# Performance work log

Hardware: AMD Instinct MI355X
Metric: run time of the kernel (lower is better)

The kernel has to match this reference:

```python
import jax, jax.numpy as jnp
import numpy as np

N_HEADS = 8
N_LAYERS = 2
LN_EPS = 1e-5


def _mha(x, Win, bin_, Wout, bout):
    # torch nn.MultiheadAttention, eval mode (dropout off). x: [b, s, d]
    b, s, d = x.shape
    dh = d // N_HEADS
    qkv = x @ Win.T + bin_                      # [b, s, 3d]
    q, k, v = jnp.split(qkv, 3, axis=-1)
    q = q.reshape(b, s, N_HEADS, dh)
    k = k.reshape(b, s, N_HEADS, dh)
    v = v.reshape(b, s, N_HEADS, dh)
    scores = jnp.einsum('bqhd,bkhd->bhqk', q, k) / jnp.sqrt(jnp.asarray(dh, x.dtype))
    attn = jax.nn.softmax(scores, axis=-1)
    o = jnp.einsum('bhqk,bkhd->bqhd', attn, v).reshape(b, s, d)
    return o @ Wout.T + bout


def _layer_norm(x, g, b):
    mu = jnp.mean(x, axis=-1, keepdims=True)
    var = jnp.mean(jnp.square(x - mu), axis=-1, keepdims=True)
    return (x - mu) * jax.lax.rsqrt(var + LN_EPS) * g + b


def _vertex_conv(feat, inc, prev, Win, bin_, Wout, bout, Wproj, ln_g, ln_b, alpha):
    # feat: [b,m,d], inc: [b,m,e]
    attn = _mha(feat, Win, bin_, Wout, bout)              # [b,m,d]
    scores = jnp.einsum('bme,bmd->bed', inc, attn)        # incidence aggregation
    w = jax.nn.softmax(scores, axis=1)                    # softmax over edges
    # fused form of einsum('bme,bmd->bmed') then einsum('bmed,bed->bed')
    edge = scores * w                                     # [b,e,d]
    edge = edge @ Wproj.T                                 # no-bias projection
    edge = _layer_norm(edge, ln_g, ln_b)
    if prev is not None:
        edge = alpha * prev + (1.0 - alpha) * edge
        edge = edge + prev
    return edge


def _edge_conv(inc, edge_feat, prev, Win, bin_, Wout, bout, Wproj, ln_g, ln_b, alpha):
    # inc: [b,m,e], edge_feat: [b,e,d]
    _ = _mha(edge_feat, Win, bin_, Wout, bout)            # attn computed, output unused downstream
    wef = jnp.einsum('bed,bme->bmd', edge_feat, inc)      # edge->node aggregation
    node = wef @ Wproj.T
    node = _layer_norm(node, ln_g, ln_b)
    if prev is not None:
        node = alpha * prev + (1.0 - alpha) * node
        node = node + prev
    return node


def setup_inputs() -> dict:
    key = jax.random.key(0)
    ks = jax.random.split(key, 8)
    b, m, e, d = 8, 1024, 1536, 256
    s = 0.02
    return {
        'features': jax.random.normal(ks[0], (b, m, d), jnp.float32),
        'inc_mat': (jax.random.uniform(ks[1], (b, m, e), jnp.float32) < 0.05).astype(jnp.float32),
        'vc_Win': jax.random.normal(ks[2], (3 * d, d), jnp.float32) * s,
        'vc_bin': jnp.zeros((3 * d,), jnp.float32),
        'vc_Wout': jax.random.normal(ks[3], (d, d), jnp.float32) * s,
        'vc_bout': jnp.zeros((d,), jnp.float32),
        'vc_Wproj': jax.random.normal(ks[4], (d, d), jnp.float32) * s,
        'vc_ln_g': jnp.ones((d,), jnp.float32),
        'vc_ln_b': jnp.zeros((d,), jnp.float32),
        'vc_alpha': jnp.asarray(0.5, jnp.float32),
        'ec_Win': jax.random.normal(ks[5], (3 * d, d), jnp.float32) * s,
        'ec_bin': jnp.zeros((3 * d,), jnp.float32),
        'ec_Wout': jax.random.normal(ks[6], (d, d), jnp.float32) * s,
        'ec_bout': jnp.zeros((d,), jnp.float32),
        'ec_Wproj': jax.random.normal(ks[7], (d, d), jnp.float32) * s,
        'ec_ln_g': jnp.ones((d,), jnp.float32),
        'ec_ln_b': jnp.zeros((d,), jnp.float32),
        'ec_alpha': jnp.asarray(0.5, jnp.float32),
    }


def reference(features, inc_mat,
              vc_Win, vc_bin, vc_Wout, vc_bout, vc_Wproj, vc_ln_g, vc_ln_b, vc_alpha,
              ec_Win, ec_bin, ec_Wout, ec_bout, ec_Wproj, ec_ln_g, ec_ln_b, ec_alpha):
    vc = (vc_Win, vc_bin, vc_Wout, vc_bout, vc_Wproj, vc_ln_g, vc_ln_b, vc_alpha)
    ec = (ec_Win, ec_bin, ec_Wout, ec_bout, ec_Wproj, ec_ln_g, ec_ln_b, ec_alpha)
    edge_feats = _vertex_conv(features, inc_mat, None, *vc)
    node_feats = _edge_conv(inc_mat, edge_feats, features, *ec)
    for _ in range(N_LAYERS):  # shared weights across layers, as in the torch module
        edge_feats = _vertex_conv(features, inc_mat, edge_feats, *vc)
        node_feats = _edge_conv(inc_mat, edge_feats, node_feats, *ec)
    return node_feats, edge_feats, inc_mat
```

## Files before the change

### kernel.cpp

```cpp
#include <hip/hip_runtime.h>
#include <stdint.h>


#define DEV static __device__ __forceinline__

typedef __attribute__((ext_vector_type(8))) short bf16x8;
typedef __attribute__((ext_vector_type(4))) float f32x4;

DEV uint16_t f2bf(float x){
  union{float f; uint32_t u;} v; v.f=x;
  uint32_t r = v.u + 0x7fffu + ((v.u>>16)&1u);
  return (uint16_t)(r>>16);
}
DEV float bf2f(uint16_t b){
  union{uint32_t u; float f;} v; v.u=((uint32_t)b)<<16; return v.f;
}

DEV uint32_t cvtpk_bf16(float lo, float hi){
  uint32_t d;
  asm("v_cvt_pk_bf16_f32 %0, %1, %2" : "=v"(d) : "v"(lo), "v"(hi));
  return d;
}

#if __has_builtin(__builtin_amdgcn_exp2f)
DEV float exp2fast(float x){ return __builtin_amdgcn_exp2f(x); }
#else
DEV float exp2fast(float x){ return __expf(x * 0.6931471805599453f); }
#endif

#if __has_builtin(__builtin_amdgcn_global_load_lds)
#define HAVE_GLL 1
#else
#define HAVE_GLL 0
#endif

DEV void load_lds16(const uint16_t* g, void* l){
#if HAVE_GLL
  __builtin_amdgcn_global_load_lds((const __attribute__((address_space(1))) uint32_t*)g,
                                   (__attribute__((address_space(3))) uint32_t*)l, 16, 0, 0);
#else
  *(bf16x8*)l = *(const bf16x8*)g;
#endif
}

__global__ __launch_bounds__(256, 3)
void qkv_prep(const float* __restrict__ inc, float* __restrict__ out_inc,
              uint16_t* __restrict__ incb, uint16_t* __restrict__ incT,
              const float* __restrict__ feats, const float* __restrict__ win,
              const float* __restrict__ bias, uint16_t* __restrict__ qkvb,
              const float* __restrict__ wout, const float* __restrict__ wpv,
              const float* __restrict__ wpe,
              uint16_t* __restrict__ ob_w, uint16_t* __restrict__ ov_w,
              uint16_t* __restrict__ oe_w,
              float* __restrict__ incpart){
  __shared__ union {
    struct { short As[128*32]; short Bs[128*32]; } g;
    float T[64*65];
  } sm;
  const int tid = threadIdx.x;
  const int bx = blockIdx.x;

  if (bx < 384){
    const int lane = tid & 63;
    const int w = tid >> 6;
    const int wm = w & 1, wn = w >> 1;
    const int r = lane & 15, q = lane >> 4;
    const int mtile = bx & 63, ntile = bx >> 6;
    const float* Fb = feats + (size_t)(mtile*128)*256;
    const float* Wb = win + (size_t)(ntile*128)*256;
    f32x4 acc[4][4];
#pragma unroll
    for (int i=0;i<4;++i)
#pragma unroll
      for (int j=0;j<4;++j) acc[i][j] = (f32x4){0.f,0.f,0.f,0.f};

    const int srow = tid >> 2;
    const int sblk = tid & 3;

    for (int kb = 0; kb < 256; kb += 32){
#pragma unroll
      for (int i=0;i<2;++i){
        int row = srow + 64*i;
        const float* src = Fb + (size_t)row*256 + kb + sblk*8;
        float4 a0 = *(const float4*)src;
        float4 a1 = *(const float4*)(src+4);
        union{uint32_t u[4]; bf16x8 v8;} pk;
        pk.u[0]=cvtpk_bf16(a0.x,a0.y); pk.u[1]=cvtpk_bf16(a0.z,a0.w);
        pk.u[2]=cvtpk_bf16(a1.x,a1.y); pk.u[3]=cvtpk_bf16(a1.z,a1.w);
        *(bf16x8*)&sm.g.As[row*32 + (sblk ^ (row&3))*8] = pk.v8;
      }
#pragma unroll
      for (int i=0;i<2;++i){
        int row = srow + 64*i;
        const float* src = Wb + (size_t)row*256 + kb + sblk*8;
        float4 a0 = *(const float4*)src;
        float4 a1 = *(const float4*)(src+4);
        union{uint32_t u[4]; bf16x8 v8;} pk;
        pk.u[0]=cvtpk_bf16(a0.x,a0.y); pk.u[1]=cvtpk_bf16(a0.z,a0.w);
        pk.u[2]=cvtpk_bf16(a1.x,a1.y); pk.u[3]=cvtpk_bf16(a1.z,a1.w);
        *(bf16x8*)&sm.g.Bs[row*32 + (sblk ^ (row&3))*8] = pk.v8;
      }
      __syncthreads();
      bf16x8 af[4], bfr[4];
#pragma unroll
      for (int mt=0;mt<4;++mt){
        int m = wm*64 + mt*16 + r;
        af[mt] = *(const bf16x8*)&sm.g.As[m*32 + (q ^ (m&3))*8];
      }
#pragma unroll
      for (int nt=0;nt<4;++nt){
        int n = wn*64 + nt*16 + r;
        bfr[nt] = *(const bf16x8*)&sm.g.Bs[n*32 + (q ^ (n&3))*8];
      }
#pragma unroll
      for (int mt=0;mt<4;++mt)
#pragma unroll
        for (int nt=0;nt<4;++nt)
          acc[mt][nt] = __builtin_amdgcn_mfma_f32_16x16x32_bf16(af[mt], bfr[nt], acc[mt][nt], 0,0,0);
      __syncthreads();
    }

    const int gm0 = mtile*128 + wm*64;
    const int gn0 = ntile*128 + wn*64;
#pragma unroll
    for (int mt=0;mt<4;++mt){
#pragma unroll
      for (int nt=0;nt<4;++nt){
        int gn = gn0 + nt*16 + r;
        float bv = bias[gn];
#pragma unroll
        for (int reg=0;reg<4;++reg){
          int gm = gm0 + mt*16 + q*4 + reg;
          qkvb[(size_t)gm*768 + gn] = f2bf(acc[mt][nt][reg] + bv);
        }
      }
    }
  } else if (bx < 3456){
    int p = bx - 384;
    int x = p % 24;
    int t = p / 24;
    int y = t & 15;
    int b = t >> 4;
    int c0 = x*64, r0 = y*64;
    int tx = tid & 15, ty = tid >> 4;
    size_t base = (size_t)b*1024*1536;
#pragma unroll
    for (int jj=0;jj<4;++jj){
      int rl = ty + jj*16;
      size_t idx = base + (size_t)(r0+rl)*1536 + c0 + tx*4;
      float4 v = *(const float4*)&inc[idx];
      *(float4*)&out_inc[idx] = v;
      union{uint16_t u[4]; uint64_t q64;} pk;
      pk.u[0]=f2bf(v.x); pk.u[1]=f2bf(v.y); pk.u[2]=f2bf(v.z); pk.u[3]=f2bf(v.w);
      *(uint64_t*)&incb[idx] = pk.q64;
      float* Tp = &sm.T[rl*65 + tx*4];
      Tp[0]=v.x; Tp[1]=v.y; Tp[2]=v.z; Tp[3]=v.w;
    }
    __syncthreads();
    int c = tid >> 2, ms = (tid & 3) * 16;
    size_t baseT = (size_t)b*1536*1024;
    uint16_t* dst = incT + baseT + (size_t)(c0+c)*1024 + r0 + ms;
    union{uint16_t u[8]; uint4 v4;} o0, o1;
    float csum = 0.f;
#pragma unroll
    for (int j=0;j<8;++j){ float v = sm.T[(ms+j)*65 + c]; csum += v; o0.u[j] = f2bf(v); }
#pragma unroll
    for (int j=0;j<8;++j){ float v = sm.T[(ms+8+j)*65 + c]; csum += v; o1.u[j] = f2bf(v); }
    *(uint4*)dst = o0.v4;
    *(uint4*)(dst+8) = o1.v4;
    csum += __shfl_xor(csum, 1);
    csum += __shfl_xor(csum, 2);
    if ((tid & 3) == 0)
      incpart[((size_t)(b*16 + y))*1536 + c0 + c] = csum;
  } else {
    int i = (bx - 3456)*256 + tid;
    const float* src; uint16_t* dst; int j;
    if (i < 16384){ src=wout; dst=ob_w; j=i; }
    else if (i < 32768){ src=wpv; dst=ov_w; j=i-16384; }
    else { src=wpe; dst=oe_w; j=i-32768; }
    float4 v = ((const float4*)src)[j];
    union { uint16_t u[4]; uint64_t q; } p;
    p.u[0]=f2bf(v.x); p.u[1]=f2bf(v.y); p.u[2]=f2bf(v.z); p.u[3]=f2bf(v.w);
    ((uint64_t*)dst)[j] = p.q;
  }
}

__global__ __launch_bounds__(256, 3)
void gemm_score_fused(const uint16_t* __restrict__ A,
                      const uint16_t* __restrict__ OT,
                      const uint16_t* __restrict__ woutb,
                      const float* __restrict__ bout,
                      const float* __restrict__ incpart,
                      float* __restrict__ part,
                      uint16_t* __restrict__ VE){
  __shared__ short Ws[256*64];
  __shared__ short As[32*64];
  __shared__ short As2[32*256];
  __shared__ float incsum[32];
  const int tid = threadIdx.x;
  const int lane = tid & 63;
  const int w = tid >> 6;
  const int r = lane & 15, q = lane >> 4;
  const int bx = (blockIdx.x & 7)*48 + (blockIdx.x >> 3);
  const int batch = bx / 48;
  const int etile = bx % 48;

  if (tid < 32){
    float s = 0.f;
#pragma unroll
    for (int y=0;y<16;++y)
      s += incpart[((size_t)(batch*16 + y))*1536 + etile*32 + tid];
    incsum[tid] = s;
  }

  const uint16_t* Ab = A + (size_t)(batch*1536 + etile*32)*1024;
  const uint16_t* Bb = OT + (size_t)batch*256*1024;

  f32x4 acc1[4][2];
#pragma unroll
  for (int i=0;i<4;++i)
#pragma unroll
    for (int j=0;j<2;++j) acc1[i][j] = (f32x4){0.f,0.f,0.f,0.f};

  const int srow = tid >> 3;
  const int sblk = tid & 7;

  for (int kb = 0; kb < 1024; kb += 64){
#pragma unroll
    for (int i=0;i<8;++i){
      int row = srow + 32*i;
      int lblk = sblk ^ (row & 7);
      load_lds16(Bb + (size_t)row*1024 + kb + lblk*8, (char*)Ws + i*4096 + tid*16);
    }
    { int lblk = sblk ^ (srow & 7);
      load_lds16(Ab + (size_t)srow*1024 + kb + lblk*8, (char*)As + tid*16); }
    __syncthreads();
#pragma unroll
    for (int kc=0;kc<2;++kc){
      bf16x8 af[4], bfr[2];
#pragma unroll
      for (int mt=0;mt<4;++mt){
        int j = w*64 + mt*16 + r;
        af[mt] = *(const bf16x8*)&Ws[j*64 + ((kc*4 + q) ^ (j&7))*8];
      }
#pragma unroll
      for (int nt=0;nt<2;++nt){
        int e = nt*16 + r;
        bfr[nt] = *(const bf16x8*)&As[e*64 + ((kc*4 + q) ^ (e&7))*8];
      }
#pragma unroll
      for (int mt=0;mt<4;++mt)
#pragma unroll
        for (int nt=0;nt<2;++nt)
          acc1[mt][nt] = __builtin_amdgcn_mfma_f32_16x16x32_bf16(af[mt], bfr[nt], acc1[mt][nt], 0,0,0);
    }
    __syncthreads();
  }

#pragma unroll
  for (int mt=0;mt<4;++mt){
    int J = w*8 + mt*2 + (q>>1);
#pragma unroll
    for (int nt=0;nt<2;++nt){
      int e = nt*16 + r;
      union{uint16_t u[4]; uint64_t q64;} pk;
#pragma unroll
      for (int reg=0;reg<4;++reg) pk.u[reg] = f2bf(acc1[mt][nt][reg]);
      *(uint64_t*)((char*)As2 + e*512 + ((J ^ (e&7))<<4) + ((q&1)<<3)) = pk.q64;
    }
  }

  f32x4 acc2[4][2];
#pragma unroll
  for (int i=0;i<4;++i)
#pragma unroll
    for (int j=0;j<2;++j) acc2[i][j] = (f32x4){0.f,0.f,0.f,0.f};

  for (int kb = 0; kb < 256; kb += 64){
#pragma unroll
    for (int i=0;i<8;++i){
      int row = srow + 32*i;
      int lblk = sblk ^ (row & 7);
      load_lds16(woutb + (size_t)row*256 + kb + lblk*8, (char*)Ws + i*4096 + tid*16);
    }
    __syncthreads();
#pragma unroll
    for (int kc=0;kc<2;++kc){
      bf16x8 af[4], bfr[2];
#pragma unroll
      for (int mt=0;mt<4;++mt){
        int d = w*64 + mt*16 + r;
        af[mt] = *(const bf16x8*)&Ws[d*64 + ((kc*4 + q) ^ (d&7))*8];
      }
#pragma unroll
      for (int nt=0;nt<2;++nt){
        int e = nt*16 + r;
        int Jr = (kb>>3) + kc*4 + q;
        bfr[nt] = *(const bf16x8*)((char*)As2 + e*512 + ((Jr ^ (e&7))<<4));
      }
#pragma unroll
      for (int mt=0;mt<4;++mt)
#pragma unroll
        for (int nt=0;nt<2;++nt)
          acc2[mt][nt] = __builtin_amdgcn_mfma_f32_16x16x32_bf16(af[mt], bfr[nt], acc2[mt][nt], 0,0,0);
    }
    __syncthreads();
  }

#pragma unroll
  for (int mt=0;mt<4;++mt){
    int d0 = w*64 + mt*16 + q*4;
    float4 bo = *(const float4*)&bout[d0];
    float colsum[4] = {0.f,0.f,0.f,0.f};
#pragma unroll
    for (int nt=0;nt<2;++nt){
      int e = nt*16 + r;
      const float isum = incsum[e];
      size_t er = (size_t)batch*1536 + etile*32 + e;
      union{uint16_t u[4]; uint64_t q64;} pk;
#pragma unroll
      for (int reg=0;reg<4;++reg){
        float bvv = (reg==0)?bo.x:(reg==1)?bo.y:(reg==2)?bo.z:bo.w;
        float v = acc2[mt][nt][reg] + isum*bvv;
        float ev = __expf(v);
        colsum[reg] += ev;
        pk.u[reg] = f2bf(v*ev);
      }
      *(uint64_t*)(VE + er*256 + d0) = pk.q64;
    }
#pragma unroll
    for (int reg=0;reg<4;++reg){
      float s = colsum[reg];
      s += __shfl_xor(s, 1);
      s += __shfl_xor(s, 2);
      s += __shfl_xor(s, 4);
      s += __shfl_xor(s, 8);
      if (r == 0)
        part[((size_t)(batch*48 + etile))*256 + d0 + reg] = s;
    }
  }
}

__global__ __launch_bounds__(256, 4)
void gemm_ln_edge(const uint16_t* __restrict__ SB, const uint16_t* __restrict__ B,
                  const float* __restrict__ part, const float* __restrict__ g,
                  const float* __restrict__ bb, const float* __restrict__ alpha,
                  float* __restrict__ out, uint16_t* __restrict__ baset){
  __shared__ short As[16*64];
  __shared__ short Bs[256*64];
  __shared__ float lnS[4][16], lnQ[4][16];
  __shared__ float PLinv[256];
  const int tid = threadIdx.x;
  const int lane = tid & 63;
  const int w = tid >> 6;
  const int r = lane & 15, q = lane >> 4;
  const int bx = (blockIdx.x & 7)*96 + (blockIdx.x >> 3);
  const int batch = bx / 96;

  {
    float s = 0.f;
#pragma unroll
    for (int i=0;i<48;++i) s += part[((size_t)batch*48 + i)*256 + tid];
    PLinv[tid] = 1.0f / s;
  }
  __syncthreads();

  f32x4 acc[4];
#pragma unroll
  for (int j=0;j<4;++j) acc[j] = (f32x4){0.f,0.f,0.f,0.f};

  const int srow = tid >> 3;
  const int sblk = tid & 7;

  for (int kb = 0; kb < 256; kb += 64){
    if (tid < 128){
      bf16x8 v = *(const bf16x8*)(SB + (size_t)(bx*16 + srow)*256 + kb + sblk*8);
      const float* Lp = &PLinv[kb + sblk*8];
      float xv[8];
#pragma unroll
      for (int j=0;j<8;++j) xv[j] = bf2f((uint16_t)v[j]) * Lp[j];
      union{uint32_t u[4]; bf16x8 v8;} pk;
      pk.u[0] = cvtpk_bf16(xv[0], xv[1]);
      pk.u[1] = cvtpk_bf16(xv[2], xv[3]);
      pk.u[2] = cvtpk_bf16(xv[4], xv[5]);
      pk.u[3] = cvtpk_bf16(xv[6], xv[7]);
      *(bf16x8*)&As[srow*64 + (sblk ^ (srow&7))*8] = pk.v8;
    }
#pragma unroll
    for (int i=0;i<8;++i){
      int row = srow + 32*i;
      int lblk = sblk ^ (row & 7);
      load_lds16(B + (size_t)row*256 + kb + lblk*8, (char*)Bs + i*4096 + tid*16);
    }
    __syncthreads();
#pragma unroll
    for (int kc=0;kc<2;++kc){
      bf16x8 af, bfr[4];
      { int m = r;
        af = *(const bf16x8*)&As[m*64 + ((kc*4 + q) ^ (m&7))*8]; }
#pragma unroll
      for (int nt=0;nt<4;++nt){
        int n = w*64 + nt*16 + r;
        bfr[nt] = *(const bf16x8*)&Bs[n*64 + ((kc*4 + q) ^ (n&7))*8];
      }
#pragma unroll
      for (int nt=0;nt<4;++nt)
        acc[nt] = __builtin_amdgcn_mfma_f32_16x16x32_bf16(af, bfr[nt], acc[nt], 0,0,0);
    }
    __syncthreads();
  }

  float rs[4], rq[4];
#pragma unroll
  for (int reg=0;reg<4;++reg){
    float s=0.f, s2=0.f;
#pragma unroll
    for (int nt=0;nt<4;++nt){
      float v = acc[nt][reg];
      s += v; s2 += v*v;
    }
#pragma unroll
    for (int off=1; off<16; off<<=1){ s += __shfl_xor(s,off); s2 += __shfl_xor(s2,off); }
    rs[reg]=s; rq[reg]=s2;
  }
  if (r == 0){
#pragma unroll
    for (int reg=0;reg<4;++reg){
      int row = q*4 + reg;
      lnS[w][row] = rs[reg];
      lnQ[w][row] = rq[reg];
    }
  }
  __syncthreads();

  const float c0 = 3.0f + alpha[0];
  float mu_[4], rstd_[4];
#pragma unroll
  for (int reg=0;reg<4;++reg){
    int row = q*4 + reg;
    float S = lnS[0][row]+lnS[1][row]+lnS[2][row]+lnS[3][row];
    float Q = lnQ[0][row]+lnQ[1][row]+lnQ[2][row]+lnQ[3][row];
    float mu = S * (1.f/256.f);
    float var = fmaxf(Q*(1.f/256.f) - mu*mu, 0.f);
    mu_[reg] = mu;
    rstd_[reg] = rsqrtf(var + 1e-5f);
  }

  int e0 = (bx % 96) * 16;
#pragma unroll
  for (int nt=0;nt<4;++nt){
    int gn = w*64 + nt*16 + r;
    float gv = g[gn], bv = bb[gn];
    union{uint16_t u[4]; uint64_t q64;} pk;
#pragma unroll
    for (int reg=0;reg<4;++reg){
      int row = q*4 + reg;
      size_t gm = (size_t)bx*16 + row;
      float o = ((acc[nt][reg]-mu_[reg])*rstd_[reg]*gv + bv) * c0;
      pk.u[reg] = f2bf(o);
      out[gm*256 + gn] = o;
    }
    int ee = e0 + q*4;
    *(uint64_t*)(baset + ((size_t)batch*256 + gn)*1536 + ee) = pk.q64;
  }
}

__global__ __launch_bounds__(256, 3)
void gemm_node_fused(const uint16_t* __restrict__ inc,
                     const uint16_t* __restrict__ baset,
                     const uint16_t* __restrict__ wpe,
                     const float* __restrict__ g, const float* __restrict__ bb,
                     const float* __restrict__ alpha,
                     const float* __restrict__ feats, float* __restrict__ out){
  __shared__ short Ws[256*64];
  __shared__ short As2[16*256];
  __shared__ short Is[16*64];
  const int tid = threadIdx.x;
  const int lane = tid & 63;
  const int w = tid >> 6;
  const int r = lane & 15, q = lane >> 4;
  const int bx = (blockIdx.x & 7)*64 + (blockIdx.x >> 3);
  const int batch = bx >> 6;
  const int mt0 = (bx & 63) * 16;

  const int srow = tid >> 3;
  const int sblk = tid & 7;

  const uint16_t* Bb = baset + (size_t)batch*256*1536;
  const uint16_t* Ib = inc + ((size_t)batch*1024 + mt0)*1536;

  f32x4 acc1[4];
#pragma unroll
  for (int i=0;i<4;++i) acc1[i] = (f32x4){0.f,0.f,0.f,0.f};

  for (int kb = 0; kb < 1536; kb += 64){
#pragma unroll
    for (int i=0;i<8;++i){
      int row = srow + 32*i;
      int lblk = sblk ^ (row & 7);
      load_lds16(Bb + (size_t)row*1536 + kb + lblk*8, (char*)Ws + i*4096 + tid*16);
    }
    if (tid < 128){
      int lblk = sblk ^ (srow & 7);
      load_lds16(Ib + (size_t)srow*1536 + kb + lblk*8, (char*)Is + tid*16);
    }
    __syncthreads();
#pragma unroll
    for (int kc=0;kc<2;++kc){
      bf16x8 af[4], bfr;
#pragma unroll
      for (int mt=0;mt<4;++mt){
        int d = w*64 + mt*16 + r;
        af[mt] = *(const bf16x8*)&Ws[d*64 + ((kc*4 + q) ^ (d&7))*8];
      }
      { int m = r;
        bfr = *(const bf16x8*)&Is[m*64 + ((kc*4 + q) ^ (m&7))*8]; }
#pragma unroll
      for (int mt=0;mt<4;++mt)
        acc1[mt] = __builtin_amdgcn_mfma_f32_16x16x32_bf16(af[mt], bfr, acc1[mt], 0,0,0);
    }
    __syncthreads();
  }

#pragma unroll
  for (int mt=0;mt<4;++mt){
    int j = w*8 + mt*2 + (q>>1);
    int m = r;
    union{uint16_t u[4]; uint64_t q64;} pk;
#pragma unroll
    for (int reg=0;reg<4;++reg) pk.u[reg] = f2bf(acc1[mt][reg]);
    *(uint64_t*)((char*)As2 + m*512 + ((j ^ (m&7))<<4) + ((q&1)<<3)) = pk.q64;
  }

  f32x4 acc2[4];
#pragma unroll
  for (int i=0;i<4;++i) acc2[i] = (f32x4){0.f,0.f,0.f,0.f};

  for (int kb = 0; kb < 256; kb += 64){
#pragma unroll
    for (int i=0;i<8;++i){
      int row = srow + 32*i;
      int lblk = sblk ^ (row & 7);
      load_lds16(wpe + (size_t)row*256 + kb + lblk*8, (char*)Ws + i*4096 + tid*16);
    }
    __syncthreads();
#pragma unroll
    for (int kc=0;kc<2;++kc){
      bf16x8 af[4], bfr;
#pragma unroll
      for (int mt=0;mt<4;++mt){
        int dp = w*64 + mt*16 + r;
        af[mt] = *(const bf16x8*)&Ws[dp*64 + ((kc*4 + q) ^ (dp&7))*8];
      }
      { int m = r;
        int jr = (kb>>3) + kc*4 + q;
        bfr = *(const bf16x8*)((char*)As2 + m*512 + ((jr ^ (m&7))<<4)); }
#pragma unroll
      for (int mt=0;mt<4;++mt)
        acc2[mt] = __builtin_amdgcn_mfma_f32_16x16x32_bf16(af[mt], bfr, acc2[mt], 0,0,0);
    }
    __syncthreads();
  }

  float* lnS = (float*)Is;
  float* lnQ = lnS + 64;
  float s_, q_;
  {
    float s=0.f, s2=0.f;
#pragma unroll
    for (int mt=0;mt<4;++mt)
#pragma unroll
      for (int reg=0;reg<4;++reg){
        float v = acc2[mt][reg];
        s += v; s2 += v*v;
      }
    s += __shfl_xor(s,16); s2 += __shfl_xor(s2,16);
    s += __shfl_xor(s,32); s2 += __shfl_xor(s2,32);
    s_ = s; q_ = s2;
  }
  if (q == 0){
    lnS[w*16 + r] = s_;
    lnQ[w*16 + r] = q_;
  }
  __syncthreads();

  const float a = alpha[0];
  const float ap1 = 1.f + a;
  const float cn = (1.f - a)*(ap1*ap1 + ap1 + 1.f);
  const float cf = ap1*ap1*ap1;

  float mu_, rstd_;
  {
    int col = r;
    float S = lnS[col] + lnS[16+col] + lnS[32+col] + lnS[48+col];
    float Q = lnQ[col] + lnQ[16+col] + lnQ[32+col] + lnQ[48+col];
    float mu = S * (1.f/256.f);
    float var = fmaxf(Q*(1.f/256.f) - mu*mu, 0.f);
    mu_ = mu;
    rstd_ = rsqrtf(var + 1e-5f);
  }

#pragma unroll
  for (int mt=0;mt<4;++mt){
    int dp0 = w*64 + mt*16 + q*4;
    float4 gv = *(const float4*)&g[dp0];
    float4 bv = *(const float4*)&bb[dp0];
    int m = r;
    size_t gm = (size_t)batch*1024 + mt0 + m;
    float4 fv = *(const float4*)&feats[gm*256 + dp0];
    float4 ov;
    ov.x = cf*fv.x + cn*((acc2[mt][0]-mu_)*rstd_*gv.x + bv.x);
    ov.y = cf*fv.y + cn*((acc2[mt][1]-mu_)*rstd_*gv.y + bv.y);
    ov.z = cf*fv.z + cn*((acc2[mt][2]-mu_)*rstd_*gv.z + bv.z);
    ov.w = cf*fv.w + cn*((acc2[mt][3]-mu_)*rstd_*gv.w + bv.w);
    *(float4*)&out[gm*256 + dp0] = ov;
  }
}

DEV void stage_K(short* Kl, const uint16_t* __restrict__ qkv, size_t rowbase,
                 int c, int h, int kr){
  const uint16_t* kp = qkv + ((rowbase + c*256 + kr)*768 + 256 + h*32);
  int sz = (kr&3) ^ ((kr>>2)&1);
#pragma unroll
  for (int lb=0; lb<4; ++lb){
    bf16x8 v = *(const bf16x8*)(kp + lb*8);
    *(bf16x8*)&Kl[kr*32 + ((lb ^ sz))*8] = v;
  }
}

DEV void stage_V(short* VT, const uint16_t* __restrict__ qkv, size_t rowbase,
                 int c, int h, int t){
  int kvp = (t>>1)*2;
  int dhh = (t&1)*16;
  const uint16_t* v0 = qkv + ((rowbase + c*256 + kvp)*768 + 512 + h*32 + dhh);
  const uint16_t* v1 = v0 + 768;
  bf16x8 a0 = *(const bf16x8*)(v0);
  bf16x8 a1 = *(const bf16x8*)(v0+8);
  bf16x8 b0 = *(const bf16x8*)(v1);
  bf16x8 b1 = *(const bf16x8*)(v1+8);
  int blkbase = kvp>>3, off = kvp&7;
#pragma unroll
  for (int i=0;i<8;++i){
    int dh = dhh + i;
    uint32_t pack = (uint32_t)(uint16_t)a0[i] | ((uint32_t)(uint16_t)b0[i]<<16);
    *(uint32_t*)&VT[dh*256 + ((blkbase ^ (dh&7))*8) + off] = pack;
  }
#pragma unroll
  for (int i=0;i<8;++i){
    int dh = dhh + 8 + i;
    uint32_t pack = (uint32_t)(uint16_t)a1[i] | ((uint32_t)(uint16_t)b1[i]<<16);
    *(uint32_t*)&VT[dh*256 + ((blkbase ^ (dh&7))*8) + off] = pack;
  }
}

__global__ __launch_bounds__(512)
void attn_fwd(const uint16_t* __restrict__ qkv, uint16_t* __restrict__ OT){
  __shared__ short Kl[256*32];
  __shared__ short VT[32*256];
  __shared__ short Pl[8][16*36];
  const int tid = threadIdx.x, lane = tid&63, w = tid>>6;
  const int r = lane&15, q = lane>>4;
  const int logical = (blockIdx.x & 7)*64 + (blockIdx.x >> 3);
  const int bh = logical >> 3, qc = logical & 7;
  const int b = bh>>3, h = bh&7;
  const int q0 = qc*128 + w*16;
  const size_t rowbase = (size_t)b*1024;

  bf16x8 aq;
  {
    const float qscale = 0.25505654380651023f;
    const uint16_t* p = qkv + ((rowbase + q0 + r)*768 + h*32 + q*8);
    bf16x8 t = *(const bf16x8*)p;
#pragma unroll
    for (int j=0;j<8;++j)
      t[j] = (short)f2bf(bf2f((uint16_t)t[j]) * qscale);
    aq = t;
  }

  f32x4 o[2];
  o[0]=(f32x4){0.f,0.f,0.f,0.f}; o[1]=(f32x4){0.f,0.f,0.f,0.f};
  float l = 0.f;

  for (int c=0;c<4;++c){
    __syncthreads();
    if (tid < 256) stage_K(Kl, qkv, rowbase, c, h, tid);
    else           stage_V(VT, qkv, rowbase, c, h, tid-256);
    __syncthreads();
    for (int s32=0; s32<8; ++s32){
#pragma unroll
      for (int t2=0;t2<2;++t2){
        int rn = s32*32 + t2*16 + r;
        int sz = (rn&3) ^ ((rn>>2)&1);
        bf16x8 bk = *(const bf16x8*)&Kl[rn*32 + ((q ^ sz))*8];
        f32x4 z = (f32x4){0.f,0.f,0.f,0.f};
        __builtin_amdgcn_s_setprio(1);
        f32x4 st = __builtin_amdgcn_mfma_f32_16x16x32_bf16(bk, aq, z, 0,0,0);
        __builtin_amdgcn_s_setprio(0);
        float p0 = exp2fast(st[0]);
        float p1 = exp2fast(st[1]);
        float p2 = exp2fast(st[2]);
        float p3 = exp2fast(st[3]);
        l += (p0+p1)+(p2+p3);
        union{uint32_t u[2]; uint64_t q64;} pk;
        pk.u[0] = cvtpk_bf16(p0, p1);
        pk.u[1] = cvtpk_bf16(p2, p3);
        *(uint64_t*)&Pl[w][r*36 + t2*16 + q*4] = pk.q64;
      }
      bf16x8 bv[2];
#pragma unroll
      for (int db=0;db<2;++db){
        int dh = db*16 + r;
        bv[db] = *(const bf16x8*)&VT[dh*256 + (((s32*4 + q) ^ (dh&7)))*8];
      }
      bf16x8 ap = *(const bf16x8*)&Pl[w][r*36 + q*8];
      __builtin_amdgcn_s_setprio(1);
#pragma unroll
      for (int db=0;db<2;++db)
        o[db] = __builtin_amdgcn_mfma_f32_16x16x32_bf16(ap, bv[db], o[db], 0,0,0);
      __builtin_amdgcn_s_setprio(0);
    }
  }

  l += __shfl_xor(l, 16);
  l += __shfl_xor(l, 32);

  short* Ob = &Pl[0][0];
  __syncthreads();
#pragma unroll
  for (int db=0; db<2; ++db){
    union{uint16_t u[4]; uint64_t q64;} pk;
#pragma unroll
    for (int reg=0;reg<4;++reg){
      float li = __shfl(l, q*4 + reg);
      pk.u[reg] = f2bf(o[db][reg] / li);
    }
    int j = db*16 + r;
    int u = w*4 + q;
    *(uint64_t*)((char*)Ob + j*256 + ((u ^ ((j&7)<<2))<<3)) = pk.q64;
  }
  __syncthreads();
  {
    int row = tid >> 4, i = tid & 15;
    uint4 v = *(const uint4*)((char*)Ob + row*256 + (((2*i) ^ ((row&7)<<2))<<3));
    *(uint4*)&OT[((size_t)(b*256 + h*32 + row))*1024 + qc*128 + i*8] = v;
  }
}

extern "C" void kernel_launch(void* const* d_in, const int* in_sizes, int n_in,
                              void* d_out, int out_size, void* d_ws, size_t ws_size,
                              hipStream_t stream){
  const float* features = (const float*)d_in[0];
  const float* inc      = (const float*)d_in[1];
  const float* vc_Win   = (const float*)d_in[2];
  const float* vc_bin   = (const float*)d_in[3];
  const float* vc_Wout  = (const float*)d_in[4];
  const float* vc_bout  = (const float*)d_in[5];
  const float* vc_Wproj = (const float*)d_in[6];
  const float* vc_ln_g  = (const float*)d_in[7];
  const float* vc_ln_b  = (const float*)d_in[8];
  const float* vc_alpha = (const float*)d_in[9];
  const float* ec_Wproj = (const float*)d_in[14];
  const float* ec_ln_g  = (const float*)d_in[15];
  const float* ec_ln_b  = (const float*)d_in[16];
  const float* ec_alpha = (const float*)d_in[17];

  float* out = (float*)d_out;
  float* out_node = out;
  float* out_edge = out + 2097152;
  float* out_inc  = out + 5242880;

  char* ws = (char*)d_ws;
  float*    PART   = (float*)   (ws + 0);
  float*    INCPART= (float*)   (ws + 1048576);
  uint16_t* WOUTB  = (uint16_t*)(ws + 4587520);
  uint16_t* WPVB   = (uint16_t*)(ws + 4718592);
  uint16_t* WPEB   = (uint16_t*)(ws + 4849664);
  uint16_t* INCB   = (uint16_t*)(ws + 4988928);
  uint16_t* INCT   = (uint16_t*)(ws + 30154752);
  uint16_t* QKVB   = (uint16_t*)(ws + 55320576);
  uint16_t* SCORESB= (uint16_t*)(ws + 55320576);
  uint16_t* OT     = (uint16_t*)(ws + 67903488);
  uint16_t* BASET  = (uint16_t*)(ws + 82583552);

  qkv_prep<<<3648,256,0,stream>>>(inc, out_inc, INCB, INCT,
                                  features, vc_Win, vc_bin, QKVB,
                                  vc_Wout, vc_Wproj, ec_Wproj,
                                  WOUTB, WPVB, WPEB, INCPART);

  attn_fwd<<<512,512,0,stream>>>(QKVB, OT);

  gemm_score_fused<<<384,256,0,stream>>>(INCT, OT, WOUTB, vc_bout,
                                         INCPART, PART, SCORESB);

  gemm_ln_edge<<<768,256,0,stream>>>(SCORESB, WPVB, PART, vc_ln_g, vc_ln_b,
                                     vc_alpha, out_edge, BASET);

  gemm_node_fused<<<512,256,0,stream>>>(INCB, BASET, WPEB, ec_ln_g, ec_ln_b,
                                        ec_alpha, features, out_node);
}
```

Measured before the change: 243.6 us.

## Move incidence cast/transpose blocks from QKV kernel into attention kernel launch

The incidence-matrix copy, bf16 cast, transpose and column-sum work is moved out of the QKV projection kernel and merged into the attention kernel as extra blocks, reshaped for 512-thread blocks. The bandwidth-bound incidence pass can then run alongside the compute-bound attention blocks instead of alongside the small QKV GEMM. The attention kernel now uses a shared-memory union, which may change occupancy, and block scheduling order decides how much real overlap happens.

```diff
diff --git a/kernel.cpp b/kernel.cpp
--- a/kernel.cpp
+++ b/kernel.cpp
@@ -44,19 +44,14 @@
 }
 
 __global__ __launch_bounds__(256, 3)
-void qkv_prep(const float* __restrict__ inc, float* __restrict__ out_inc,
-              uint16_t* __restrict__ incb, uint16_t* __restrict__ incT,
-              const float* __restrict__ feats, const float* __restrict__ win,
+void qkv_cast(const float* __restrict__ feats, const float* __restrict__ win,
               const float* __restrict__ bias, uint16_t* __restrict__ qkvb,
               const float* __restrict__ wout, const float* __restrict__ wpv,
               const float* __restrict__ wpe,
               uint16_t* __restrict__ ob_w, uint16_t* __restrict__ ov_w,
-              uint16_t* __restrict__ oe_w,
-              float* __restrict__ incpart){
-  __shared__ union {
-    struct { short As[128*32]; short Bs[128*32]; } g;
-    float T[64*65];
-  } sm;
+              uint16_t* __restrict__ oe_w){
+  __shared__ short As[128*32];
+  __shared__ short Bs[128*32];
   const int tid = threadIdx.x;
   const int bx = blockIdx.x;
 
@@ -87,7 +82,7 @@
         union{uint32_t u[4]; bf16x8 v8;} pk;
         pk.u[0]=cvtpk_bf16(a0.x,a0.y); pk.u[1]=cvtpk_bf16(a0.z,a0.w);
         pk.u[2]=cvtpk_bf16(a1.x,a1.y); pk.u[3]=cvtpk_bf16(a1.z,a1.w);
-        *(bf16x8*)&sm.g.As[row*32 + (sblk ^ (row&3))*8] = pk.v8;
+        *(bf16x8*)&As[row*32 + (sblk ^ (row&3))*8] = pk.v8;
       }
 #pragma unroll
       for (int i=0;i<2;++i){
@@ -98,19 +93,19 @@
         union{uint32_t u[4]; bf16x8 v8;} pk;
         pk.u[0]=cvtpk_bf16(a0.x,a0.y); pk.u[1]=cvtpk_bf16(a0.z,a0.w);
         pk.u[2]=cvtpk_bf16(a1.x,a1.y); pk.u[3]=cvtpk_bf16(a1.z,a1.w);
-        *(bf16x8*)&sm.g.Bs[row*32 + (sblk ^ (row&3))*8] = pk.v8;
+        *(bf16x8*)&Bs[row*32 + (sblk ^ (row&3))*8] = pk.v8;
       }
       __syncthreads();
       bf16x8 af[4], bfr[4];
 #pragma unroll
       for (int mt=0;mt<4;++mt){
         int m = wm*64 + mt*16 + r;
-        af[mt] = *(const bf16x8*)&sm.g.As[m*32 + (q ^ (m&3))*8];
+        af[mt] = *(const bf16x8*)&As[m*32 + (q ^ (m&3))*8];
       }
 #pragma unroll
       for (int nt=0;nt<4;++nt){
         int n = wn*64 + nt*16 + r;
-        bfr[nt] = *(const bf16x8*)&sm.g.Bs[n*32 + (q ^ (n&3))*8];
+        bfr[nt] = *(const bf16x8*)&Bs[n*32 + (q ^ (n&3))*8];
       }
 #pragma unroll
       for (int mt=0;mt<4;++mt)
@@ -135,8 +130,69 @@
         }
       }
     }
-  } else if (bx < 3456){
-    int p = bx - 384;
+  } else {
+    int i = (bx - 384)*256 + tid;
+    const float* src; uint16_t* dst; int j;
+    if (i < 16384){ src=wout; dst=ob_w; j=i; }
+    else if (i < 32768){ src=wpv; dst=ov_w; j=i-16384; }
+    else { src=wpe; dst=oe_w; j=i-32768; }
+    float4 v = ((const float4*)src)[j];
+    union { uint16_t u[4]; uint64_t q; } p;
+    p.u[0]=f2bf(v.x); p.u[1]=f2bf(v.y); p.u[2]=f2bf(v.z); p.u[3]=f2bf(v.w);
+    ((uint64_t*)dst)[j] = p.q;
+  }
+}
+
+DEV void stage_K(short* Kl, const uint16_t* __restrict__ qkv, size_t rowbase,
+                 int c, int h, int kr){
+  const uint16_t* kp = qkv + ((rowbase + c*256 + kr)*768 + 256 + h*32);
+  int sz = (kr&3) ^ ((kr>>2)&1);
+#pragma unroll
+  for (int lb=0; lb<4; ++lb){
+    bf16x8 v = *(const bf16x8*)(kp + lb*8);
+    *(bf16x8*)&Kl[kr*32 + ((lb ^ sz))*8] = v;
+  }
+}
+
+DEV void stage_V(short* VT, const uint16_t* __restrict__ qkv, size_t rowbase,
+                 int c, int h, int t){
+  int kvp = (t>>1)*2;
+  int dhh = (t&1)*16;
+  const uint16_t* v0 = qkv + ((rowbase + c*256 + kvp)*768 + 512 + h*32 + dhh);
+  const uint16_t* v1 = v0 + 768;
+  bf16x8 a0 = *(const bf16x8*)(v0);
+  bf16x8 a1 = *(const bf16x8*)(v0+8);
+  bf16x8 b0 = *(const bf16x8*)(v1);
+  bf16x8 b1 = *(const bf16x8*)(v1+8);
+  int blkbase = kvp>>3, off = kvp&7;
+#pragma unroll
+  for (int i=0;i<8;++i){
+    int dh = dhh + i;
+    uint32_t pack = (uint32_t)(uint16_t)a0[i] | ((uint32_t)(uint16_t)b0[i]<<16);
+    *(uint32_t*)&VT[dh*256 + ((blkbase ^ (dh&7))*8) + off] = pack;
+  }
+#pragma unroll
+  for (int i=0;i<8;++i){
+    int dh = dhh + 8 + i;
+    uint32_t pack = (uint32_t)(uint16_t)a1[i] | ((uint32_t)(uint16_t)b1[i]<<16);
+    *(uint32_t*)&VT[dh*256 + ((blkbase ^ (dh&7))*8) + off] = pack;
+  }
+}
+
+__global__ __launch_bounds__(512)
+void attn_prep(const uint16_t* __restrict__ qkv, uint16_t* __restrict__ OT,
+               const float* __restrict__ inc, float* __restrict__ out_inc,
+               uint16_t* __restrict__ incb, uint16_t* __restrict__ incT,
+               float* __restrict__ incpart){
+  __shared__ union {
+    struct { short Kl[256*32]; short VT[32*256]; short Pl[8][16*36]; } a;
+    float T[64*65];
+  } sm;
+  const int tid = threadIdx.x;
+  const int bx = blockIdx.x;
+
+  if (bx >= 512){
+    int p = bx - 512;
     int x = p % 24;
     int t = p / 24;
     int y = t & 15;
@@ -145,8 +201,8 @@
     int tx = tid & 15, ty = tid >> 4;
     size_t base = (size_t)b*1024*1536;
 #pragma unroll
-    for (int jj=0;jj<4;++jj){
-      int rl = ty + jj*16;
+    for (int jj=0;jj<2;++jj){
+      int rl = ty + jj*32;
       size_t idx = base + (size_t)(r0+rl)*1536 + c0 + tx*4;
       float4 v = *(const float4*)&inc[idx];
       *(float4*)&out_inc[idx] = v;
@@ -157,31 +213,109 @@
       Tp[0]=v.x; Tp[1]=v.y; Tp[2]=v.z; Tp[3]=v.w;
     }
     __syncthreads();
-    int c = tid >> 2, ms = (tid & 3) * 16;
+    int c = tid >> 3, msel = tid & 7, ms = msel*8;
     size_t baseT = (size_t)b*1536*1024;
     uint16_t* dst = incT + baseT + (size_t)(c0+c)*1024 + r0 + ms;
-    union{uint16_t u[8]; uint4 v4;} o0, o1;
+    union{uint16_t u[8]; uint4 v4;} o0;
     float csum = 0.f;
 #pragma unroll
     for (int j=0;j<8;++j){ float v = sm.T[(ms+j)*65 + c]; csum += v; o0.u[j] = f2bf(v); }
-#pragma unroll
-    for (int j=0;j<8;++j){ float v = sm.T[(ms+8+j)*65 + c]; csum += v; o1.u[j] = f2bf(v); }
     *(uint4*)dst = o0.v4;
-    *(uint4*)(dst+8) = o1.v4;
     csum += __shfl_xor(csum, 1);
     csum += __shfl_xor(csum, 2);
-    if ((tid & 3) == 0)
+    csum += __shfl_xor(csum, 4);
+    if (msel == 0)
       incpart[((size_t)(b*16 + y))*1536 + c0 + c] = csum;
-  } else {
-    int i = (bx - 3456)*256 + tid;
-    const float* src; uint16_t* dst; int j;
-    if (i < 16384){ src=wout; dst=ob_w; j=i; }
-    else if (i < 32768){ src=wpv; dst=ov_w; j=i-16384; }
-    else { src=wpe; dst=oe_w; j=i-32768; }
-    float4 v = ((const float4*)src)[j];
-    union { uint16_t u[4]; uint64_t q; } p;
-    p.u[0]=f2bf(v.x); p.u[1]=f2bf(v.y); p.u[2]=f2bf(v.z); p.u[3]=f2bf(v.w);
-    ((uint64_t*)dst)[j] = p.q;
+    return;
+  }
+
+  short* Kl = sm.a.Kl;
+  short* VT = sm.a.VT;
+  const int lane = tid&63, w = tid>>6;
+  const int r = lane&15, q = lane>>4;
+  const int logical = (bx & 7)*64 + (bx >> 3);
+  const int bh = logical >> 3, qc = logical & 7;
+  const int b = bh>>3, h = bh&7;
+  const int q0 = qc*128 + w*16;
+  const size_t rowbase = (size_t)b*1024;
+
+  bf16x8 aq;
+  {
+    const float qscale = 0.25505654380651023f;
+    const uint16_t* p = qkv + ((rowbase + q0 + r)*768 + h*32 + q*8);
+    bf16x8 t = *(const bf16x8*)p;
+#pragma unroll
+    for (int j=0;j<8;++j)
+      t[j] = (short)f2bf(bf2f((uint16_t)t[j]) * qscale);
+    aq = t;
+  }
+
+  f32x4 o[2];
+  o[0]=(f32x4){0.f,0.f,0.f,0.f}; o[1]=(f32x4){0.f,0.f,0.f,0.f};
+  float l = 0.f;
+
+  for (int c=0;c<4;++c){
+    __syncthreads();
+    if (tid < 256) stage_K(Kl, qkv, rowbase, c, h, tid);
+    else           stage_V(VT, qkv, rowbase, c, h, tid-256);
+    __syncthreads();
+    for (int s32=0; s32<8; ++s32){
+#pragma unroll
+      for (int t2=0;t2<2;++t2){
+        int rn = s32*32 + t2*16 + r;
+        int sz = (rn&3) ^ ((rn>>2)&1);
+        bf16x8 bk = *(const bf16x8*)&Kl[rn*32 + ((q ^ sz))*8];
+        f32x4 z = (f32x4){0.f,0.f,0.f,0.f};
+        __builtin_amdgcn_s_setprio(1);
+        f32x4 st = __builtin_amdgcn_mfma_f32_16x16x32_bf16(bk, aq, z, 0,0,0);
+        __builtin_amdgcn_s_setprio(0);
+        float p0 = exp2fast(st[0]);
+        float p1 = exp2fast(st[1]);
+        float p2 = exp2fast(st[2]);
+        float p3 = exp2fast(st[3]);
+        l += (p0+p1)+(p2+p3);
+        union{uint32_t u[2]; uint64_t q64;} pk;
+        pk.u[0] = cvtpk_bf16(p0, p1);
+        pk.u[1] = cvtpk_bf16(p2, p3);
+        *(uint64_t*)&sm.a.Pl[w][r*36 + t2*16 + q*4] = pk.q64;
+      }
+      bf16x8 bv[2];
+#pragma unroll
+      for (int db=0;db<2;++db){
+        int dh = db*16 + r;
+        bv[db] = *(const bf16x8*)&VT[dh*256 + (((s32*4 + q) ^ (dh&7)))*8];
+      }
+      bf16x8 ap = *(const bf16x8*)&sm.a.Pl[w][r*36 + q*8];
+      __builtin_amdgcn_s_setprio(1);
+#pragma unroll
+      for (int db=0;db<2;++db)
+        o[db] = __builtin_amdgcn_mfma_f32_16x16x32_bf16(ap, bv[db], o[db], 0,0,0);
+      __builtin_amdgcn_s_setprio(0);
+    }
+  }
+
+  l += __shfl_xor(l, 16);
+  l += __shfl_xor(l, 32);
+
+  short* Ob = &sm.a.Pl[0][0];
+  __syncthreads();
+#pragma unroll
+  for (int db=0; db<2; ++db){
+    union{uint16_t u[4]; uint64_t q64;} pk;
+#pragma unroll
+    for (int reg=0;reg<4;++reg){
+      float li = __shfl(l, q*4 + reg);
+      pk.u[reg] = f2bf(o[db][reg] / li);
+    }
+    int j = db*16 + r;
+    int u = w*4 + q;
+    *(uint64_t*)((char*)Ob + j*256 + ((u ^ ((j&7)<<2))<<3)) = pk.q64;
+  }
+  __syncthreads();
+  {
+    int row = tid >> 4, i = tid & 15;
+    uint4 v = *(const uint4*)((char*)Ob + row*256 + (((2*i) ^ ((row&7)<<2))<<3));
+    *(uint4*)&OT[((size_t)(b*256 + h*32 + row))*1024 + qc*128 + i*8] = v;
   }
 }
 
@@ -617,135 +751,6 @@
   }
 }
 
-DEV void stage_K(short* Kl, const uint16_t* __restrict__ qkv, size_t rowbase,
-                 int c, int h, int kr){
-  const uint16_t* kp = qkv + ((rowbase + c*256 + kr)*768 + 256 + h*32);
-  int sz = (kr&3) ^ ((kr>>2)&1);
-#pragma unroll
-  for (int lb=0; lb<4; ++lb){
-    bf16x8 v = *(const bf16x8*)(kp + lb*8);
-    *(bf16x8*)&Kl[kr*32 + ((lb ^ sz))*8] = v;
-  }
-}
-
-DEV void stage_V(short* VT, const uint16_t* __restrict__ qkv, size_t rowbase,
-                 int c, int h, int t){
-  int kvp = (t>>1)*2;
-  int dhh = (t&1)*16;
-  const uint16_t* v0 = qkv + ((rowbase + c*256 + kvp)*768 + 512 + h*32 + dhh);
-  const uint16_t* v1 = v0 + 768;
-  bf16x8 a0 = *(const bf16x8*)(v0);
-  bf16x8 a1 = *(const bf16x8*)(v0+8);
-  bf16x8 b0 = *(const bf16x8*)(v1);
-  bf16x8 b1 = *(const bf16x8*)(v1+8);
-  int blkbase = kvp>>3, off = kvp&7;
-#pragma unroll
-  for (int i=0;i<8;++i){
-    int dh = dhh + i;
-    uint32_t pack = (uint32_t)(uint16_t)a0[i] | ((uint32_t)(uint16_t)b0[i]<<16);
-    *(uint32_t*)&VT[dh*256 + ((blkbase ^ (dh&7))*8) + off] = pack;
-  }
-#pragma unroll
-  for (int i=0;i<8;++i){
-    int dh = dhh + 8 + i;
-    uint32_t pack = (uint32_t)(uint16_t)a1[i] | ((uint32_t)(uint16_t)b1[i]<<16);
-    *(uint32_t*)&VT[dh*256 + ((blkbase ^ (dh&7))*8) + off] = pack;
-  }
-}
-
-__global__ __launch_bounds__(512)
-void attn_fwd(const uint16_t* __restrict__ qkv, uint16_t* __restrict__ OT){
-  __shared__ short Kl[256*32];
-  __shared__ short VT[32*256];
-  __shared__ short Pl[8][16*36];
-  const int tid = threadIdx.x, lane = tid&63, w = tid>>6;
-  const int r = lane&15, q = lane>>4;
-  const int logical = (blockIdx.x & 7)*64 + (blockIdx.x >> 3);
-  const int bh = logical >> 3, qc = logical & 7;
-  const int b = bh>>3, h = bh&7;
-  const int q0 = qc*128 + w*16;
-  const size_t rowbase = (size_t)b*1024;
-
-  bf16x8 aq;
-  {
-    const float qscale = 0.25505654380651023f;
-    const uint16_t* p = qkv + ((rowbase + q0 + r)*768 + h*32 + q*8);
-    bf16x8 t = *(const bf16x8*)p;
-#pragma unroll
-    for (int j=0;j<8;++j)
-      t[j] = (short)f2bf(bf2f((uint16_t)t[j]) * qscale);
-    aq = t;
-  }
-
-  f32x4 o[2];
-  o[0]=(f32x4){0.f,0.f,0.f,0.f}; o[1]=(f32x4){0.f,0.f,0.f,0.f};
-  float l = 0.f;
-
-  for (int c=0;c<4;++c){
-    __syncthreads();
-    if (tid < 256) stage_K(Kl, qkv, rowbase, c, h, tid);
-    else           stage_V(VT, qkv, rowbase, c, h, tid-256);
-    __syncthreads();
-    for (int s32=0; s32<8; ++s32){
-#pragma unroll
-      for (int t2=0;t2<2;++t2){
-        int rn = s32*32 + t2*16 + r;
-        int sz = (rn&3) ^ ((rn>>2)&1);
-        bf16x8 bk = *(const bf16x8*)&Kl[rn*32 + ((q ^ sz))*8];
-        f32x4 z = (f32x4){0.f,0.f,0.f,0.f};
-        __builtin_amdgcn_s_setprio(1);
-        f32x4 st = __builtin_amdgcn_mfma_f32_16x16x32_bf16(bk, aq, z, 0,0,0);
-        __builtin_amdgcn_s_setprio(0);
-        float p0 = exp2fast(st[0]);
-        float p1 = exp2fast(st[1]);
-        float p2 = exp2fast(st[2]);
-        float p3 = exp2fast(st[3]);
-        l += (p0+p1)+(p2+p3);
-        union{uint32_t u[2]; uint64_t q64;} pk;
-        pk.u[0] = cvtpk_bf16(p0, p1);
-        pk.u[1] = cvtpk_bf16(p2, p3);
-        *(uint64_t*)&Pl[w][r*36 + t2*16 + q*4] = pk.q64;
-      }
-      bf16x8 bv[2];
-#pragma unroll
-      for (int db=0;db<2;++db){
-        int dh = db*16 + r;
-        bv[db] = *(const bf16x8*)&VT[dh*256 + (((s32*4 + q) ^ (dh&7)))*8];
-      }
-      bf16x8 ap = *(const bf16x8*)&Pl[w][r*36 + q*8];
-      __builtin_amdgcn_s_setprio(1);
-#pragma unroll
-      for (int db=0;db<2;++db)
-        o[db] = __builtin_amdgcn_mfma_f32_16x16x32_bf16(ap, bv[db], o[db], 0,0,0);
-      __builtin_amdgcn_s_setprio(0);
-    }
-  }
-
-  l += __shfl_xor(l, 16);
-  l += __shfl_xor(l, 32);
-
-  short* Ob = &Pl[0][0];
-  __syncthreads();
-#pragma unroll
-  for (int db=0; db<2; ++db){
-    union{uint16_t u[4]; uint64_t q64;} pk;
-#pragma unroll
-    for (int reg=0;reg<4;++reg){
-      float li = __shfl(l, q*4 + reg);
-      pk.u[reg] = f2bf(o[db][reg] / li);
-    }
-    int j = db*16 + r;
-    int u = w*4 + q;
-    *(uint64_t*)((char*)Ob + j*256 + ((u ^ ((j&7)<<2))<<3)) = pk.q64;
-  }
-  __syncthreads();
-  {
-    int row = tid >> 4, i = tid & 15;
-    uint4 v = *(const uint4*)((char*)Ob + row*256 + (((2*i) ^ ((row&7)<<2))<<3));
-    *(uint4*)&OT[((size_t)(b*256 + h*32 + row))*1024 + qc*128 + i*8] = v;
-  }
-}
-
 extern "C" void kernel_launch(void* const* d_in, const int* in_sizes, int n_in,
                               void* d_out, int out_size, void* d_ws, size_t ws_size,
                               hipStream_t stream){
@@ -782,12 +787,12 @@
   uint16_t* OT     = (uint16_t*)(ws + 67903488);
   uint16_t* BASET  = (uint16_t*)(ws + 82583552);
 
-  qkv_prep<<<3648,256,0,stream>>>(inc, out_inc, INCB, INCT,
-                                  features, vc_Win, vc_bin, QKVB,
-                                  vc_Wout, vc_Wproj, ec_Wproj,
-                                  WOUTB, WPVB, WPEB, INCPART);
-
-  attn_fwd<<<512,512,0,stream>>>(QKVB, OT);
+  qkv_cast<<<576,256,0,stream>>>(features, vc_Win, vc_bin, QKVB,
+                                 vc_Wout, vc_Wproj, ec_Wproj,
+                                 WOUTB, WPVB, WPEB);
+
+  attn_prep<<<3584,512,0,stream>>>(QKVB, OT, inc, out_inc, INCB, INCT,
+                                   INCPART);
 
   gemm_score_fused<<<384,256,0,stream>>>(INCT, OT, WOUTB, vc_bout,
                                          INCPART, PART, SCORESB);
```

Result: no change. 245.4 us (+0.8%).
